# Optimization experiments

Hardware: AMD Instinct MI355X
Metric: run time of the kernel (lower is better)

The kernel has to match this reference:

```python
import jax, jax.numpy as jnp
import numpy as np
from jax import lax

N, H, BS = 256, 1024, 128
ALPHA, BETA, SIGMA = 60.0, 20.0, 5.0
EPS = 1e-8


def _mlp_w(key, n_in, n_out):
    return jax.random.normal(key, (n_out, n_in), dtype=jnp.float32) / np.sqrt(n_in)


def setup_inputs() -> dict:
    key = jax.random.key(0)
    ks = jax.random.split(key, 8)
    inp = {
        "t": jnp.zeros((), dtype=jnp.float32),
        "x": jax.random.normal(ks[0], (BS, N), dtype=jnp.float32),
        "Wf1": _mlp_w(ks[1], N, H), "bf1": jnp.zeros((H,), jnp.float32),
        "Wf2": _mlp_w(ks[2], H, N), "bf2": jnp.zeros((N,), jnp.float32),
        "Wg1": _mlp_w(ks[3], N, H), "bg1": jnp.zeros((H,), jnp.float32),
        "Wg2": _mlp_w(ks[4], H, N), "bg2": jnp.zeros((N,), jnp.float32),
        "Wk1": _mlp_w(ks[5], N, H), "bk1": jnp.zeros((H,), jnp.float32),
        "Wk2": _mlp_w(ks[6], H, N), "bk2": jnp.zeros((N,), jnp.float32),
    }
    return inp


def reference(t, x, Wf1, bf1, Wf2, bf2, Wg1, bg1, Wg2, bg2, Wk1, bk1, Wk2, bk2):
    def mlp(u, W1, b1, W2, b2):
        return jnp.tanh(u @ W1.T + b1) @ W2.T + b2

    def k_func(u):
        return mlp(u, Wk1, bk1, Wk2, bk2)

    f_out = mlp(x, Wf1, bf1, Wf2, bf2)          # f_model(t, x); t unused
    k_out = k_func(x)
    G_k_out = mlp(x, Wg1, bg1, Wg2, bg2)        # g_fn(x)[0]
    dx_dt = f_out + G_k_out

    # compute_k_jacobian: torch detaches u, so no grad flows to x here.
    # torch layout: J[b, j, i] = d k_i / d u_j  (transpose of jacfwd output)
    x_d = lax.stop_gradient(x)
    J_fwd = jax.vmap(jax.jacfwd(k_func))(x_d)   # [bs, i_out, j_in]
    J_x = jnp.swapaxes(J_fwd, 1, 2)             # [bs, j, i]

    k_norm = jnp.linalg.norm(k_out, axis=1)                      # [bs]
    Jf = jnp.einsum('bji,bi->bj', J_x, f_out)                    # bmm(J, f)
    Jf_norm = jnp.linalg.norm(Jf, axis=1)
    c1 = Jf_norm - ALPHA * k_norm ** (2 * SIGMA - 1)
    JG = jnp.einsum('bji,bi->bj', J_x, G_k_out)                  # bmm(J, G)
    c2 = jnp.sum(k_out * JG, axis=1) - BETA * k_norm ** (2 * SIGMA)

    mask = (c1 > EPS) | (c2 < -EPS)                              # [bs]
    dx_upd = jnp.where(mask[:, None], jnp.zeros_like(dx_dt), dx_dt)
    return (dx_upd + dx_dt) / 2
```

## Files before the change

### kernel.cpp

```cpp
#include <hip/hip_runtime.h>
#include <stdint.h>

#define N_ 256
#define H_ 1024
#define BS_ 128

#define WS_SK    0
#define WS_OACC  131072
#define WS_OPART 229376
#define WS_JPART 1802240
#define WS_FLOATS 2850816

__global__ __launch_bounds__(256) void k12_l1l2(
    const float* __restrict__ x,
    const float* __restrict__ Wf1, const float* __restrict__ bf1,
    const float* __restrict__ Wg1, const float* __restrict__ bg1,
    const float* __restrict__ Wk1, const float* __restrict__ bk1,
    const float* __restrict__ Wf2, const float* __restrict__ bf2,
    const float* __restrict__ Wg2, const float* __restrict__ bg2,
    const float* __restrict__ Wk2, const float* __restrict__ bk2,
    float* __restrict__ sk, float* __restrict__ opart)
{
    const int bx = blockIdx.x;
    const int g  = bx % 48;
    const int rt = bx / 48;
    const int m  = g >> 4;
    const int ht = g & 15;
    const int t  = threadIdx.x;
    const int h0 = ht * 64;
    const int r0 = rt * 8;

    const float* W1 = (m == 0) ? Wf1 : (m == 1) ? Wg1 : Wk1;
    const float* b1 = (m == 0) ? bf1 : (m == 1) ? bg1 : bk1;
    const float* W2 = (m == 0) ? Wf2 : (m == 1) ? Wg2 : Wk2;
    const float* b2 = (m == 0) ? bf2 : (m == 1) ? bg2 : bk2;

    __shared__ float xs[8][256];
    __shared__ float ts[8][64];
    for (int u = t; u < 2048; u += 256)
        xs[u >> 8][u & 255] = x[(r0 + (u >> 8)) * N_ + (u & 255)];
    __syncthreads();

    {
        const int hl = t & 63;
        const int rg = (t >> 6) * 2;
        const int h  = h0 + hl;
        float a0 = b1[h], a1 = a0;
        const float4* w4  = (const float4*)(W1 + h * N_);
        const float4* xa4 = (const float4*)xs[rg];
        const float4* xb4 = (const float4*)xs[rg + 1];
        #pragma unroll 8
        for (int c = 0; c < 64; ++c) {
            float4 w = w4[c];
            float4 a = xa4[c];
            float4 b = xb4[c];
            a0 += w.x * a.x + w.y * a.y + w.z * a.z + w.w * a.w;
            a1 += w.x * b.x + w.y * b.y + w.z * b.z + w.w * b.w;
        }
        const float v0 = tanhf(a0), v1 = tanhf(a1);
        ts[rg][hl]     = v0;
        ts[rg + 1][hl] = v1;
        if (m == 2) {
            sk[(r0 + rg) * H_ + h]     = 1.0f - v0 * v0;
            sk[(r0 + rg + 1) * H_ + h] = 1.0f - v1 * v1;
        }
    }
    __syncthreads();

    {
        float acc[8];
        const float bv = (ht == 0) ? b2[t] : 0.0f;
        #pragma unroll
        for (int r = 0; r < 8; ++r) acc[r] = bv;

        const float4* w4 = (const float4*)(W2 + t * H_ + h0);
        #pragma unroll 4
        for (int c = 0; c < 16; ++c) {
            float4 w = w4[c];
            #pragma unroll
            for (int r = 0; r < 8; ++r) {
                float4 a = ((const float4*)ts[r])[c];
                acc[r] += w.x * a.x + w.y * a.y + w.z * a.z + w.w * a.w;
            }
        }
        #pragma unroll
        for (int r = 0; r < 8; ++r)
            opart[((ht * 3 + m) * BS_ + r0 + r) * N_ + t] = acc[r];
    }
}

__global__ __launch_bounds__(256) void k25_reduce(
    const float* __restrict__ opart, float* __restrict__ oacc)
{
    const int tid = blockIdx.x * 256 + threadIdx.x;
    float s = 0.f;
    #pragma unroll
    for (int ks = 0; ks < 16; ++ks)
        s += opart[ks * (3 * BS_ * N_) + tid];
    oacc[tid] = s;
}

__global__ __launch_bounds__(256) void k3_vj(
    const float* __restrict__ Wk1, const float* __restrict__ Wk2,
    const float* __restrict__ oacc, const float* __restrict__ sk,
    float* __restrict__ jpart)
{
    const int q  = blockIdx.x & 15;
    const int rp = blockIdx.x >> 4;
    const int t  = threadIdx.x;
    const int r0 = rp * 4;
    const int h0 = q * 64;

    __shared__ float sfv[4][64], sgv[4][64];

    {
        const int hl = t & 63;
        const int rl = __builtin_amdgcn_readfirstlane(t >> 6);
        const int h  = h0 + hl;
        const float* fo_p = oacc + (r0 + rl) * N_;
        const float* go_p = oacc + (BS_ + r0 + rl) * N_;
        const float* w2   = Wk2 + h;
        float vf = 0.f, vg = 0.f;
        #pragma unroll 8
        for (int c = 0; c < 64; ++c) {
            const float4 of = *(const float4*)(fo_p + 4 * c);
            const float4 og = *(const float4*)(go_p + 4 * c);
            const float w0 = w2[(4 * c + 0) * H_];
            const float w1 = w2[(4 * c + 1) * H_];
            const float w2v = w2[(4 * c + 2) * H_];
            const float w3 = w2[(4 * c + 3) * H_];
            vf += of.x * w0 + of.y * w1 + of.z * w2v + of.w * w3;
            vg += og.x * w0 + og.y * w1 + og.z * w2v + og.w * w3;
        }
        const float s = sk[(r0 + rl) * H_ + h];
        sfv[rl][hl] = s * vf;
        sgv[rl][hl] = s * vg;
    }
    __syncthreads();

    {
        float jf[4] = {0.f, 0.f, 0.f, 0.f};
        float jg[4] = {0.f, 0.f, 0.f, 0.f};
        const float* w1 = Wk1 + h0 * N_ + t;
        #pragma unroll 4
        for (int c = 0; c < 16; ++c) {
            const float w0 = w1[(4 * c + 0) * N_];
            const float wv1 = w1[(4 * c + 1) * N_];
            const float wv2 = w1[(4 * c + 2) * N_];
            const float wv3 = w1[(4 * c + 3) * N_];
            #pragma unroll
            for (int r = 0; r < 4; ++r) {
                const float4 sf = ((const float4*)sfv[r])[c];
                const float4 sg = ((const float4*)sgv[r])[c];
                jf[r] += sf.x * w0 + sf.y * wv1 + sf.z * wv2 + sf.w * wv3;
                jg[r] += sg.x * w0 + sg.y * wv1 + sg.z * wv2 + sg.w * wv3;
            }
        }
        #pragma unroll
        for (int r = 0; r < 4; ++r) {
            jpart[((q * 2 + 0) * BS_ + r0 + r) * N_ + t] = jf[r];
            jpart[((q * 2 + 1) * BS_ + r0 + r) * N_ + t] = jg[r];
        }
    }
}

__global__ __launch_bounds__(256) void k4_final(
    const float* __restrict__ oacc,
    const float* __restrict__ jpart,
    float* __restrict__ out)
{
    const int r = blockIdx.x;
    const int t = threadIdx.x;
    __shared__ float red[12];

    const float fo = oacc[r * N_ + t];
    const float go = oacc[(BS_ + r) * N_ + t];
    const float ko = oacc[(2 * BS_ + r) * N_ + t];

    float jf = 0.f, jg = 0.f;
    #pragma unroll
    for (int q = 0; q < 16; ++q) {
        jf += jpart[((q * 2 + 0) * BS_ + r) * N_ + t];
        jg += jpart[((q * 2 + 1) * BS_ + r) * N_ + t];
    }

    float v0 = ko * ko, v1 = jf * jf, v2 = ko * jg;
    #pragma unroll
    for (int o = 32; o > 0; o >>= 1) {
        v0 += __shfl_xor(v0, o, 64);
        v1 += __shfl_xor(v1, o, 64);
        v2 += __shfl_xor(v2, o, 64);
    }
    const int wid = t >> 6;
    if ((t & 63) == 0) {
        red[wid * 3 + 0] = v0;
        red[wid * 3 + 1] = v1;
        red[wid * 3 + 2] = v2;
    }
    __syncthreads();
    const float kn2 = red[0] + red[3] + red[6] + red[9];
    const float jf2 = red[1] + red[4] + red[7] + red[10];
    const float kjg = red[2] + red[5] + red[8] + red[11];

    const float knorm = sqrtf(kn2);
    const float kn4 = kn2 * kn2;
    const float kn8 = kn4 * kn4;
    const float c1 = sqrtf(jf2) - 60.0f * kn8 * knorm;
    const float c2 = kjg - 20.0f * kn8 * kn2;
    const float scale = ((c1 > 1e-8f) || (c2 < -1e-8f)) ? 0.5f : 1.0f;

    out[r * N_ + t] = (fo + go) * scale;
}

__global__ __launch_bounds__(256) void manifold_fused(
    const float* __restrict__ x,
    const float* __restrict__ Wf1, const float* __restrict__ bf1v,
    const float* __restrict__ Wf2, const float* __restrict__ bf2v,
    const float* __restrict__ Wg1, const float* __restrict__ bg1v,
    const float* __restrict__ Wg2, const float* __restrict__ bg2v,
    const float* __restrict__ Wk1, const float* __restrict__ bk1v,
    const float* __restrict__ Wk2, const float* __restrict__ bk2v,
    float* __restrict__ out)
{
    const int b = blockIdx.x;
    const int t = threadIdx.x;
    __shared__ float xs[N_];
    __shared__ float tf[H_], tg[H_], tk[H_], sk[H_];
    __shared__ float fo[N_], go[N_];
    __shared__ float sfv[H_], sgv[H_];
    __shared__ float red[12];

    xs[t] = x[b * N_ + t];
    __syncthreads();
    {
        float acc[12];
        const float4* rows[12];
        #pragma unroll
        for (int m = 0; m < 4; ++m) {
            const int h = t + m * 256;
            rows[m]     = (const float4*)(Wf1 + h * N_);
            rows[4 + m] = (const float4*)(Wg1 + h * N_);
            rows[8 + m] = (const float4*)(Wk1 + h * N_);
            acc[m] = bf1v[h]; acc[4 + m] = bg1v[h]; acc[8 + m] = bk1v[h];
        }
        const float4* xs4 = (const float4*)xs;
        #pragma unroll 2
        for (int c = 0; c < 64; ++c) {
            float4 a = xs4[c];
            #pragma unroll
            for (int r = 0; r < 12; ++r) {
                float4 w = rows[r][c];
                acc[r] += w.x * a.x + w.y * a.y + w.z * a.z + w.w * a.w;
            }
        }
        #pragma unroll
        for (int m = 0; m < 4; ++m) {
            const int h = t + m * 256;
            float vtf = tanhf(acc[m]);
            float vtg = tanhf(acc[4 + m]);
            float vtk = tanhf(acc[8 + m]);
            tf[h] = vtf; tg[h] = vtg; tk[h] = vtk; sk[h] = 1.0f - vtk * vtk;
        }
    }
    __syncthreads();
    float af = bf2v[t], ag = bg2v[t], ak = bk2v[t];
    {
        const float4* rf = (const float4*)(Wf2 + t * H_);
        const float4* rg = (const float4*)(Wg2 + t * H_);
        const float4* rk = (const float4*)(Wk2 + t * H_);
        #pragma unroll 2
        for (int c = 0; c < 256; ++c) {
            float4 wf = rf[c], wg = rg[c], wk = rk[c];
            float4 vf = ((const float4*)tf)[c];
            af += wf.x*vf.x + wf.y*vf.y + wf.z*vf.z + wf.w*vf.w;
            float4 vg = ((const float4*)tg)[c];
            ag += wg.x*vg.x + wg.y*vg.y + wg.z*vg.z + wg.w*vg.w;
            float4 vk = ((const float4*)tk)[c];
            ak += wk.x*vk.x + wk.y*vk.y + wk.z*vk.z + wk.w*vk.w;
        }
    }
    fo[t] = af; go[t] = ag;
    __syncthreads();
    {
        float vf[4] = {0.f,0.f,0.f,0.f}, vg[4] = {0.f,0.f,0.f,0.f};
        const float* base = Wk2 + 4 * t;
        #pragma unroll 4
        for (int i = 0; i < N_; ++i) {
            float4 w = *(const float4*)(base + i * H_);
            float fv = fo[i], gv = go[i];
            vf[0]+=w.x*fv; vf[1]+=w.y*fv; vf[2]+=w.z*fv; vf[3]+=w.w*fv;
            vg[0]+=w.x*gv; vg[1]+=w.y*gv; vg[2]+=w.z*gv; vg[3]+=w.w*gv;
        }
        #pragma unroll
        for (int c = 0; c < 4; ++c) {
            sfv[4*t+c] = sk[4*t+c]*vf[c];
            sgv[4*t+c] = sk[4*t+c]*vg[c];
        }
    }
    __syncthreads();
    float jf = 0.f, jg = 0.f;
    {
        const float* col = Wk1 + t;
        #pragma unroll 4
        for (int c = 0; c < 256; ++c) {
            float4 s4 = ((const float4*)sfv)[c];
            float4 g4 = ((const float4*)sgv)[c];
            const int h = c * 4;
            float w0 = col[(h+0)*N_], w1 = col[(h+1)*N_];
            float w2 = col[(h+2)*N_], w3 = col[(h+3)*N_];
            jf += s4.x*w0 + s4.y*w1 + s4.z*w2 + s4.w*w3;
            jg += g4.x*w0 + g4.y*w1 + g4.z*w2 + g4.w*w3;
        }
    }
    float v0 = ak*ak, v1 = jf*jf, v2 = ak*jg;
    #pragma unroll
    for (int o = 32; o > 0; o >>= 1) {
        v0 += __shfl_xor(v0, o, 64);
        v1 += __shfl_xor(v1, o, 64);
        v2 += __shfl_xor(v2, o, 64);
    }
    const int wid = t >> 6;
    if ((t & 63) == 0) {
        red[wid*3+0] = v0; red[wid*3+1] = v1; red[wid*3+2] = v2;
    }
    __syncthreads();
    const float kn2 = red[0]+red[3]+red[6]+red[9];
    const float jf2 = red[1]+red[4]+red[7]+red[10];
    const float kjg = red[2]+red[5]+red[8]+red[11];
    const float knorm = sqrtf(kn2);
    const float kn4 = kn2*kn2, kn8 = kn4*kn4;
    const float c1 = sqrtf(jf2) - 60.0f*kn8*knorm;
    const float c2 = kjg - 20.0f*kn8*kn2;
    const float scale = ((c1 > 1e-8f) || (c2 < -1e-8f)) ? 0.5f : 1.0f;
    out[b*N_+t] = (af+ag)*scale;
}

extern "C" void kernel_launch(void* const* d_in, const int* in_sizes, int n_in,
                              void* d_out, int out_size, void* d_ws, size_t ws_size,
                              hipStream_t stream) {
    const float* x    = (const float*)d_in[1];
    const float* Wf1  = (const float*)d_in[2];
    const float* bf1v = (const float*)d_in[3];
    const float* Wf2  = (const float*)d_in[4];
    const float* bf2v = (const float*)d_in[5];
    const float* Wg1  = (const float*)d_in[6];
    const float* bg1v = (const float*)d_in[7];
    const float* Wg2  = (const float*)d_in[8];
    const float* bg2v = (const float*)d_in[9];
    const float* Wk1  = (const float*)d_in[10];
    const float* bk1v = (const float*)d_in[11];
    const float* Wk2  = (const float*)d_in[12];
    const float* bk2v = (const float*)d_in[13];
    float* out = (float*)d_out;

    if (ws_size < (size_t)WS_FLOATS * sizeof(float)) {
        manifold_fused<<<BS_, 256, 0, stream>>>(
            x, Wf1, bf1v, Wf2, bf2v, Wg1, bg1v, Wg2, bg2v,
            Wk1, bk1v, Wk2, bk2v, out);
        return;
    }

    float* ws    = (float*)d_ws;
    float* sk    = ws + WS_SK;
    float* oacc  = ws + WS_OACC;
    float* opart = ws + WS_OPART;
    float* jpart = ws + WS_JPART;

    k12_l1l2  <<<768, 256, 0, stream>>>(x, Wf1, bf1v, Wg1, bg1v, Wk1, bk1v,
                                        Wf2, bf2v, Wg2, bg2v, Wk2, bk2v,
                                        sk, opart);
    k25_reduce<<<384, 256, 0, stream>>>(opart, oacc);
    k3_vj     <<<512, 256, 0, stream>>>(Wk1, Wk2, oacc, sk, jpart);
    k4_final  <<<BS_, 256, 0, stream>>>(oacc, jpart, out);
}
```

Measured before the change: 135.4 us.

## Fold split-K reduction into consumers and double row tile in MLP kernel

Removes the separate reduction kernel by having k3_vj and k4_final sum the 16 hidden-tile partials of the MLP outputs directly from opart, with k3 staging the reduced f/g rows in shared memory. The first kernel now processes 16 batch rows per block instead of 8, halving the grid to 384 blocks and reusing each weight load across more rows. This saves one launch and the oacc round trip. The cost is redundant partial-sum reads across k3 blocks (16 q-blocks per row group), higher register and LDS pressure in k12, and fewer blocks for occupancy.

```diff
diff --git a/kernel.cpp b/kernel.cpp
--- a/kernel.cpp
+++ b/kernel.cpp
@@ -6,10 +6,9 @@
 #define BS_ 128
 
 #define WS_SK    0
-#define WS_OACC  131072
-#define WS_OPART 229376
-#define WS_JPART 1802240
-#define WS_FLOATS 2850816
+#define WS_OPART 131072
+#define WS_JPART 1703936
+#define WS_FLOATS 2752512
 
 __global__ __launch_bounds__(256) void k12_l1l2(
     const float* __restrict__ x,
@@ -28,81 +27,79 @@
     const int ht = g & 15;
     const int t  = threadIdx.x;
     const int h0 = ht * 64;
-    const int r0 = rt * 8;
+    const int r0 = rt * 16;
 
     const float* W1 = (m == 0) ? Wf1 : (m == 1) ? Wg1 : Wk1;
     const float* b1 = (m == 0) ? bf1 : (m == 1) ? bg1 : bk1;
     const float* W2 = (m == 0) ? Wf2 : (m == 1) ? Wg2 : Wk2;
     const float* b2 = (m == 0) ? bf2 : (m == 1) ? bg2 : bk2;
 
-    __shared__ float xs[8][256];
-    __shared__ float ts[8][64];
-    for (int u = t; u < 2048; u += 256)
+    __shared__ float xs[16][256];
+    __shared__ float ts[16][64];
+    for (int u = t; u < 4096; u += 256)
         xs[u >> 8][u & 255] = x[(r0 + (u >> 8)) * N_ + (u & 255)];
     __syncthreads();
 
     {
         const int hl = t & 63;
-        const int rg = (t >> 6) * 2;
+        const int rq = (t >> 6) * 4;
         const int h  = h0 + hl;
-        float a0 = b1[h], a1 = a0;
+        float a0 = b1[h], a1 = a0, a2 = a0, a3 = a0;
         const float4* w4  = (const float4*)(W1 + h * N_);
-        const float4* xa4 = (const float4*)xs[rg];
-        const float4* xb4 = (const float4*)xs[rg + 1];
+        const float4* x0 = (const float4*)xs[rq];
+        const float4* x1 = (const float4*)xs[rq + 1];
+        const float4* x2 = (const float4*)xs[rq + 2];
+        const float4* x3 = (const float4*)xs[rq + 3];
         #pragma unroll 8
         for (int c = 0; c < 64; ++c) {
             float4 w = w4[c];
-            float4 a = xa4[c];
-            float4 b = xb4[c];
-            a0 += w.x * a.x + w.y * a.y + w.z * a.z + w.w * a.w;
-            a1 += w.x * b.x + w.y * b.y + w.z * b.z + w.w * b.w;
+            float4 p = x0[c];
+            a0 += w.x * p.x + w.y * p.y + w.z * p.z + w.w * p.w;
+            float4 q = x1[c];
+            a1 += w.x * q.x + w.y * q.y + w.z * q.z + w.w * q.w;
+            float4 r = x2[c];
+            a2 += w.x * r.x + w.y * r.y + w.z * r.z + w.w * r.w;
+            float4 s = x3[c];
+            a3 += w.x * s.x + w.y * s.y + w.z * s.z + w.w * s.w;
         }
         const float v0 = tanhf(a0), v1 = tanhf(a1);
-        ts[rg][hl]     = v0;
-        ts[rg + 1][hl] = v1;
+        const float v2 = tanhf(a2), v3 = tanhf(a3);
+        ts[rq][hl] = v0; ts[rq + 1][hl] = v1;
+        ts[rq + 2][hl] = v2; ts[rq + 3][hl] = v3;
         if (m == 2) {
-            sk[(r0 + rg) * H_ + h]     = 1.0f - v0 * v0;
-            sk[(r0 + rg + 1) * H_ + h] = 1.0f - v1 * v1;
-        }
-    }
-    __syncthreads();
-
-    {
-        float acc[8];
+            sk[(r0 + rq) * H_ + h]     = 1.0f - v0 * v0;
+            sk[(r0 + rq + 1) * H_ + h] = 1.0f - v1 * v1;
+            sk[(r0 + rq + 2) * H_ + h] = 1.0f - v2 * v2;
+            sk[(r0 + rq + 3) * H_ + h] = 1.0f - v3 * v3;
+        }
+    }
+    __syncthreads();
+
+    {
+        float acc[16];
         const float bv = (ht == 0) ? b2[t] : 0.0f;
         #pragma unroll
-        for (int r = 0; r < 8; ++r) acc[r] = bv;
+        for (int r = 0; r < 16; ++r) acc[r] = bv;
 
         const float4* w4 = (const float4*)(W2 + t * H_ + h0);
-        #pragma unroll 4
+        #pragma unroll 2
         for (int c = 0; c < 16; ++c) {
             float4 w = w4[c];
             #pragma unroll
-            for (int r = 0; r < 8; ++r) {
+            for (int r = 0; r < 16; ++r) {
                 float4 a = ((const float4*)ts[r])[c];
                 acc[r] += w.x * a.x + w.y * a.y + w.z * a.z + w.w * a.w;
             }
         }
         #pragma unroll
-        for (int r = 0; r < 8; ++r)
+        for (int r = 0; r < 16; ++r)
             opart[((ht * 3 + m) * BS_ + r0 + r) * N_ + t] = acc[r];
     }
-}
-
-__global__ __launch_bounds__(256) void k25_reduce(
-    const float* __restrict__ opart, float* __restrict__ oacc)
-{
-    const int tid = blockIdx.x * 256 + threadIdx.x;
-    float s = 0.f;
-    #pragma unroll
-    for (int ks = 0; ks < 16; ++ks)
-        s += opart[ks * (3 * BS_ * N_) + tid];
-    oacc[tid] = s;
 }
 
 __global__ __launch_bounds__(256) void k3_vj(
     const float* __restrict__ Wk1, const float* __restrict__ Wk2,
-    const float* __restrict__ oacc, const float* __restrict__ sk,
+    const float* __restrict__ opart, const float* __restrict__ sk,
     float* __restrict__ jpart)
 {
     const int q  = blockIdx.x & 15;
@@ -111,20 +108,32 @@
     const int r0 = rp * 4;
     const int h0 = q * 64;
 
+    __shared__ float fos[4][256], gos[4][256];
     __shared__ float sfv[4][64], sgv[4][64];
 
+    for (int u = t; u < 1024; u += 256) {
+        const int r = u >> 8, i = u & 255;
+        float s0 = 0.f, s1 = 0.f;
+        #pragma unroll
+        for (int ks = 0; ks < 16; ++ks) {
+            s0 += opart[((ks * 3 + 0) * BS_ + r0 + r) * N_ + i];
+            s1 += opart[((ks * 3 + 1) * BS_ + r0 + r) * N_ + i];
+        }
+        fos[r][i] = s0;
+        gos[r][i] = s1;
+    }
+    __syncthreads();
+
     {
         const int hl = t & 63;
-        const int rl = __builtin_amdgcn_readfirstlane(t >> 6);
+        const int rl = t >> 6;
         const int h  = h0 + hl;
-        const float* fo_p = oacc + (r0 + rl) * N_;
-        const float* go_p = oacc + (BS_ + r0 + rl) * N_;
-        const float* w2   = Wk2 + h;
+        const float* w2 = Wk2 + h;
         float vf = 0.f, vg = 0.f;
         #pragma unroll 8
         for (int c = 0; c < 64; ++c) {
-            const float4 of = *(const float4*)(fo_p + 4 * c);
-            const float4 og = *(const float4*)(go_p + 4 * c);
+            const float4 of = ((const float4*)fos[rl])[c];
+            const float4 og = ((const float4*)gos[rl])[c];
             const float w0 = w2[(4 * c + 0) * H_];
             const float w1 = w2[(4 * c + 1) * H_];
             const float w2v = w2[(4 * c + 2) * H_];
@@ -165,7 +174,7 @@
 }
 
 __global__ __launch_bounds__(256) void k4_final(
-    const float* __restrict__ oacc,
+    const float* __restrict__ opart,
     const float* __restrict__ jpart,
     float* __restrict__ out)
 {
@@ -173,9 +182,13 @@
     const int t = threadIdx.x;
     __shared__ float red[12];
 
-    const float fo = oacc[r * N_ + t];
-    const float go = oacc[(BS_ + r) * N_ + t];
-    const float ko = oacc[(2 * BS_ + r) * N_ + t];
+    float fo = 0.f, go = 0.f, ko = 0.f;
+    #pragma unroll
+    for (int ks = 0; ks < 16; ++ks) {
+        fo += opart[((ks * 3 + 0) * BS_ + r) * N_ + t];
+        go += opart[((ks * 3 + 1) * BS_ + r) * N_ + t];
+        ko += opart[((ks * 3 + 2) * BS_ + r) * N_ + t];
+    }
 
     float jf = 0.f, jg = 0.f;
     #pragma unroll
@@ -362,14 +375,12 @@
 
     float* ws    = (float*)d_ws;
     float* sk    = ws + WS_SK;
-    float* oacc  = ws + WS_OACC;
     float* opart = ws + WS_OPART;
     float* jpart = ws + WS_JPART;
 
-    k12_l1l2  <<<768, 256, 0, stream>>>(x, Wf1, bf1v, Wg1, bg1v, Wk1, bk1v,
-                                        Wf2, bf2v, Wg2, bg2v, Wk2, bk2v,
-                                        sk, opart);
-    k25_reduce<<<384, 256, 0, stream>>>(opart, oacc);
-    k3_vj     <<<512, 256, 0, stream>>>(Wk1, Wk2, oacc, sk, jpart);
-    k4_final  <<<BS_, 256, 0, stream>>>(oacc, jpart, out);
-}
+    k12_l1l2<<<384, 256, 0, stream>>>(x, Wf1, bf1v, Wg1, bg1v, Wk1, bk1v,
+                                      Wf2, bf2v, Wg2, bg2v, Wk2, bk2v,
+                                      sk, opart);
+    k3_vj   <<<512, 256, 0, stream>>>(Wk1, Wk2, opart, sk, jpart);
+    k4_final<<<BS_, 256, 0, stream>>>(opart, jpart, out);
+}
```

After: 131.6 us. 2.8% less time.
